# Optimization experiments

Measured on AMD Instinct MI355X. Metric: run time of the kernel, lower is better.

## Reference

```python
import jax, jax.numpy as jnp
import numpy as np

LN_EPS = 1e-5

def _layernorm(x, g, b):
    mu = jnp.mean(x, axis=-1, keepdims=True)
    var = jnp.mean((x - mu) ** 2, axis=-1, keepdims=True)
    return (x - mu) * jax.lax.rsqrt(var + LN_EPS) * g + b

def _mlp(x, w0, b0, wh, bh, lng, lnb, wout, bout):
    # Linear -> ReLU -> LN, repeated; final Linear.
    h = _layernorm(jax.nn.relu(x @ w0.T + b0), lng[0], lnb[0])
    for i in range(wh.shape[0]):
        h = _layernorm(jax.nn.relu(h @ wh[i].T + bh[i]), lng[i + 1], lnb[i + 1])
    return h @ wout.T + bout

def _vq(z, codebook, commitment_cost=0.25):
    B, A, D = z.shape
    flat = z.reshape(-1, D)                                  # [N, D]
    d = (jnp.sum(flat ** 2, axis=1, keepdims=True)
         + jnp.sum(codebook ** 2, axis=1)
         - 2.0 * flat @ codebook.T)                          # [N, K]
    idx = jnp.argmin(d, axis=1)                              # [N]
    quantized = codebook[idx].reshape(z.shape)               # gather, not one-hot matmul
    e_latent = jnp.mean((jax.lax.stop_gradient(quantized) - z) ** 2)
    q_latent = jnp.mean((quantized - jax.lax.stop_gradient(z)) ** 2)
    vq_loss = commitment_cost * e_latent + q_latent
    quantized = z + jax.lax.stop_gradient(quantized - z)     # straight-through
    return quantized, vq_loss

def setup_inputs() -> dict:
    key = jax.random.key(0)
    ks = jax.random.split(key, 8)
    H, D, K = 256, 64, 512
    B, A = 2048, 128
    s = lambda fan_in: 1.0 / np.sqrt(fan_in)
    return {
        'x': jax.random.normal(ks[0], (B, A, 3), jnp.float32),
        'enc_w0': jax.random.normal(ks[1], (H, 3), jnp.float32) * s(3),
        'enc_b0': jnp.zeros((H,), jnp.float32),
        'enc_wh': jax.random.normal(ks[2], (2, H, H), jnp.float32) * s(H),
        'enc_bh': jnp.zeros((2, H), jnp.float32),
        'enc_ln_g': jnp.ones((3, H), jnp.float32),
        'enc_ln_b': jnp.zeros((3, H), jnp.float32),
        'enc_wout': jax.random.normal(ks[3], (D, H), jnp.float32) * s(H),
        'enc_bout': jnp.zeros((D,), jnp.float32),
        'codebook': jax.random.uniform(ks[4], (K, D), jnp.float32, -1.0 / K, 1.0 / K),
        'dec_w0': jax.random.normal(ks[5], (H, D), jnp.float32) * s(D),
        'dec_b0': jnp.zeros((H,), jnp.float32),
        'dec_wh': jax.random.normal(ks[6], (2, H, H), jnp.float32) * s(H),
        'dec_bh': jnp.zeros((2, H), jnp.float32),
        'dec_ln_g': jnp.ones((3, H), jnp.float32),
        'dec_ln_b': jnp.zeros((3, H), jnp.float32),
        'dec_wout': jax.random.normal(ks[7], (3, H), jnp.float32) * s(H),
        'dec_bout': jnp.zeros((3,), jnp.float32),
    }

def reference(x, enc_w0, enc_b0, enc_wh, enc_bh, enc_ln_g, enc_ln_b, enc_wout, enc_bout,
              codebook, dec_w0, dec_b0, dec_wh, dec_bh, dec_ln_g, dec_ln_b, dec_wout, dec_bout):
    z = _mlp(x, enc_w0, enc_b0, enc_wh, enc_bh, enc_ln_g, enc_ln_b, enc_wout, enc_bout)
    quantized, vq_loss = _vq(z, codebook)
    recon = _mlp(quantized, dec_w0, dec_b0, dec_wh, dec_bh, dec_ln_g, dec_ln_b, dec_wout, dec_bout)
    loss = jnp.mean((recon - x) ** 2) + vq_loss
    return recon, quantized, loss
```

## Files before the change

### kernel.cpp

```cpp
#include <hip/hip_runtime.h>
#include <math.h>

__device__ __forceinline__ float wred(float s) {
  #pragma unroll
  for (int o = 32; o > 0; o >>= 1) s += __shfl_xor(s, o, 64);
  return s;
}

__device__ __forceinline__ float fma4(float4 w, float4 a, float acc) {
  return fmaf(w.w, a.w, fmaf(w.z, a.z, fmaf(w.y, a.y, fmaf(w.x, a.x, acc))));
}

__device__ __forceinline__ void ln_rows32(float (*A)[256], const float* __restrict__ gg,
                                          const float* __restrict__ bb, int t) {
  const int w = t >> 6, l = t & 63;
  const float g0 = gg[l], g1 = gg[l + 64], g2 = gg[l + 128], g3 = gg[l + 192];
  const float c0 = bb[l], c1 = bb[l + 64], c2 = bb[l + 128], c3 = bb[l + 192];
  #pragma unroll
  for (int rr = 0; rr < 8; ++rr) {
    const int r = w * 8 + rr;
    const float v0 = A[r][l], v1 = A[r][l + 64], v2 = A[r][l + 128], v3 = A[r][l + 192];
    float s = ((v0 + v1) + v2) + v3;
    s = wred(s);
    const float mu = s * (1.f / 256.f);
    const float d0 = v0 - mu, d1 = v1 - mu, d2 = v2 - mu, d3 = v3 - mu;
    float s2 = fmaf(d3, d3, fmaf(d2, d2, fmaf(d1, d1, d0 * d0)));
    s2 = wred(s2);
    const float var = s2 * (1.f / 256.f);
    const float rs = 1.f / sqrtf(var + 1e-5f);
    A[r][l]       = (d0 * rs) * g0 + c0;
    A[r][l + 64]  = (d1 * rs) * g1 + c1;
    A[r][l + 128] = (d2 * rs) * g2 + c2;
    A[r][l + 192] = (d3 * rs) * g3 + c3;
  }
  __syncthreads();
}

__device__ __forceinline__ void hidden_layer32(float (*A)[256], const float* __restrict__ W,
                                               const float* __restrict__ B, int t) {
  const int g = t >> 7;
  const int j0 = t & 127, j1 = j0 + 128;
  const float4* W0 = (const float4*)(W + j0 * 256);
  const float4* W1 = (const float4*)(W + j1 * 256);
  float acc0[16], acc1[16];
  #pragma unroll
  for (int r = 0; r < 16; ++r) { acc0[r] = 0.f; acc1[r] = 0.f; }
  #pragma unroll 2
  for (int kq = 0; kq < 64; ++kq) {
    const float4 wq0 = W0[kq], wq1 = W1[kq];
    #pragma unroll
    for (int rr = 0; rr < 16; ++rr) {
      const float4 a = *(const float4*)&A[g * 16 + rr][kq * 4];
      acc0[rr] = fma4(wq0, a, acc0[rr]);
      acc1[rr] = fma4(wq1, a, acc1[rr]);
    }
  }
  const float bb0 = B[j0], bb1 = B[j1];
  __syncthreads();
  #pragma unroll
  for (int rr = 0; rr < 16; ++rr) {
    const int r = g * 16 + rr;
    A[r][j0] = fmaxf(acc0[rr] + bb0, 0.f);
    A[r][j1] = fmaxf(acc1[rr] + bb1, 0.f);
  }
  __syncthreads();
}


__device__ __forceinline__ void ldw4(float4* w, const float* __restrict__ WT, int kq, int c0) {
  const float* p = WT + kq * 1024 + c0;
  w[0] = *(const float4*)(p);
  w[1] = *(const float4*)(p + 256);
  w[2] = *(const float4*)(p + 512);
  w[3] = *(const float4*)(p + 768);
}

__device__ __forceinline__ void step16(const float (*A)[256], int kq, const float4* w, float4* acc) {
  #pragma unroll
  for (int rr = 0; rr < 16; ++rr) {
    const float4 a = *(const float4*)&A[rr][kq * 4];
    float4 o = acc[rr];
    o.x = fmaf(a.x, w[0].x, o.x); o.y = fmaf(a.x, w[0].y, o.y);
    o.z = fmaf(a.x, w[0].z, o.z); o.w = fmaf(a.x, w[0].w, o.w);
    o.x = fmaf(a.y, w[1].x, o.x); o.y = fmaf(a.y, w[1].y, o.y);
    o.z = fmaf(a.y, w[1].z, o.z); o.w = fmaf(a.y, w[1].w, o.w);
    o.x = fmaf(a.z, w[2].x, o.x); o.y = fmaf(a.z, w[2].y, o.y);
    o.z = fmaf(a.z, w[2].z, o.z); o.w = fmaf(a.z, w[2].w, o.w);
    o.x = fmaf(a.w, w[3].x, o.x); o.y = fmaf(a.w, w[3].y, o.y);
    o.z = fmaf(a.w, w[3].z, o.z); o.w = fmaf(a.w, w[3].w, o.w);
    acc[rr] = o;
  }
}

__device__ __forceinline__ void hid16(const float (*A)[256], const float* __restrict__ WT,
                                      const float* __restrict__ Bp, int c0, float4* acc) {
  #pragma unroll
  for (int rr = 0; rr < 16; ++rr) acc[rr] = make_float4(0.f, 0.f, 0.f, 0.f);
  float4 wA[4], wB[4];
  ldw4(wA, WT, 0, c0);
  #pragma unroll 1
  for (int kq = 0; kq < 64; kq += 2) {
    ldw4(wB, WT, kq + 1, c0);
    step16(A, kq, wA, acc);
    if (kq + 2 < 64) ldw4(wA, WT, kq + 2, c0);
    step16(A, kq + 1, wB, acc);
  }
  const float4 bb = *(const float4*)&Bp[c0];
  #pragma unroll
  for (int rr = 0; rr < 16; ++rr) {
    acc[rr].x = fmaxf(acc[rr].x + bb.x, 0.f);
    acc[rr].y = fmaxf(acc[rr].y + bb.y, 0.f);
    acc[rr].z = fmaxf(acc[rr].z + bb.z, 0.f);
    acc[rr].w = fmaxf(acc[rr].w + bb.w, 0.f);
  }
}

__device__ __forceinline__ void ln_pad(float4* acc, float (*P)[36],
                                       const float* __restrict__ gg,
                                       const float* __restrict__ bb, int l) {
  const int c0 = l * 4;
  float p[16];
  #pragma unroll
  for (int r = 0; r < 16; ++r) {
    const float4 v = acc[r];
    p[r] = (v.x + v.y) + (v.z + v.w);
  }
  #pragma unroll
  for (int r = 0; r < 16; ++r) p[r] += __shfl_xor(p[r], 32, 64);
  __syncthreads();
  if (l < 32) {
    #pragma unroll
    for (int r = 0; r < 16; ++r) P[r][l] = p[r];
  }
  __syncthreads();
  if (l < 16) {
    float q[8];
    #pragma unroll
    for (int j = 0; j < 8; ++j) {
      const float4 u = *(const float4*)&P[l][4 * j];
      q[j] = (u.x + u.y) + (u.z + u.w);
    }
    const float s = ((q[0] + q[1]) + (q[2] + q[3])) + ((q[4] + q[5]) + (q[6] + q[7]));
    P[l][32] = s * (1.f / 256.f);
  }
  __syncthreads();
  float mu[16];
  #pragma unroll
  for (int r = 0; r < 16; ++r) mu[r] = P[r][32];
  #pragma unroll
  for (int r = 0; r < 16; ++r) {
    const float4 v = acc[r];
    const float d0 = v.x - mu[r], d1 = v.y - mu[r], d2 = v.z - mu[r], d3 = v.w - mu[r];
    p[r] = fmaf(d3, d3, fmaf(d2, d2, fmaf(d1, d1, d0 * d0)));
  }
  #pragma unroll
  for (int r = 0; r < 16; ++r) p[r] += __shfl_xor(p[r], 32, 64);
  if (l < 32) {
    #pragma unroll
    for (int r = 0; r < 16; ++r) P[r][l] = p[r];
  }
  __syncthreads();
  if (l < 16) {
    float q[8];
    #pragma unroll
    for (int j = 0; j < 8; ++j) {
      const float4 u = *(const float4*)&P[l][4 * j];
      q[j] = (u.x + u.y) + (u.z + u.w);
    }
    const float s2 = ((q[0] + q[1]) + (q[2] + q[3])) + ((q[4] + q[5]) + (q[6] + q[7]));
    const float var = s2 * (1.f / 256.f);
    P[l][33] = 1.f / sqrtf(var + 1e-5f);
  }
  __syncthreads();
  const float4 g = *(const float4*)&gg[c0];
  const float4 c = *(const float4*)&bb[c0];
  #pragma unroll
  for (int r = 0; r < 16; ++r) {
    const float rs = P[r][33];
    const float4 v = acc[r];
    acc[r].x = ((v.x - mu[r]) * rs) * g.x + c.x;
    acc[r].y = ((v.y - mu[r]) * rs) * g.y + c.y;
    acc[r].z = ((v.z - mu[r]) * rs) * g.z + c.z;
    acc[r].w = ((v.w - mu[r]) * rs) * g.w + c.w;
  }
}

__device__ __forceinline__ void storeA(float (*A)[256], const float4* acc, int c0) {
  #pragma unroll
  for (int rr = 0; rr < 16; ++rr) *(float4*)&A[rr][c0] = acc[rr];
}

__device__ __forceinline__ void out16(const float (*A)[256], const float* __restrict__ WTo,
                                      const float* __restrict__ bo, float* __restrict__ zout, int l) {
  float o[16];
  #pragma unroll
  for (int rr = 0; rr < 16; ++rr) o[rr] = 0.f;
  #pragma unroll 2
  for (int kq = 0; kq < 64; ++kq) {
    const float w0 = WTo[(kq * 4 + 0) * 64 + l];
    const float w1 = WTo[(kq * 4 + 1) * 64 + l];
    const float w2 = WTo[(kq * 4 + 2) * 64 + l];
    const float w3 = WTo[(kq * 4 + 3) * 64 + l];
    #pragma unroll
    for (int rr = 0; rr < 16; ++rr) {
      const float4 a = *(const float4*)&A[rr][kq * 4];
      o[rr] = fmaf(a.w, w3, fmaf(a.z, w2, fmaf(a.y, w1, fmaf(a.x, w0, o[rr]))));
    }
  }
  const float bb = bo[l];
  #pragma unroll
  for (int rr = 0; rr < 16; ++rr) zout[rr * 64 + l] = o[rr] + bb;
}

__global__ __launch_bounds__(64, 2) void k_enc(
    const float* __restrict__ x, const float* __restrict__ w0,
    const float* __restrict__ b0, const float* __restrict__ wt1,
    const float* __restrict__ wt2, const float* __restrict__ bh,
    const float* __restrict__ lng, const float* __restrict__ lnb,
    const float* __restrict__ wtout, const float* __restrict__ bout,
    float* __restrict__ z) {
  __shared__ float A[16][256];
  __shared__ float P[16][36];
  const int l = threadIdx.x;
  const int c0 = l * 4;
  const size_t rbase = (size_t)blockIdx.x * 16;
  float4 acc[16];

  {
    const float* wp = w0 + c0 * 3;
    float wv[12];
    #pragma unroll
    for (int i = 0; i < 12; ++i) wv[i] = wp[i];
    const float4 bb = *(const float4*)&b0[c0];
    #pragma unroll
    for (int rr = 0; rr < 16; ++rr) {
      const float x0 = x[(rbase + rr) * 3];
      const float x1 = x[(rbase + rr) * 3 + 1];
      const float x2 = x[(rbase + rr) * 3 + 2];
      acc[rr].x = fmaxf(fmaf(wv[2],  x2, fmaf(wv[1],  x1, wv[0] * x0)) + bb.x, 0.f);
      acc[rr].y = fmaxf(fmaf(wv[5],  x2, fmaf(wv[4],  x1, wv[3] * x0)) + bb.y, 0.f);
      acc[rr].z = fmaxf(fmaf(wv[8],  x2, fmaf(wv[7],  x1, wv[6] * x0)) + bb.z, 0.f);
      acc[rr].w = fmaxf(fmaf(wv[11], x2, fmaf(wv[10], x1, wv[9] * x0)) + bb.w, 0.f);
    }
  }
  ln_pad(acc, P, lng, lnb, l);
  storeA(A, acc, c0);
  __syncthreads();

  hid16(A, wt1, bh, c0, acc);
  ln_pad(acc, P, lng + 256, lnb + 256, l);
  storeA(A, acc, c0);
  __syncthreads();

  hid16(A, wt2, bh + 256, c0, acc);
  ln_pad(acc, P, lng + 512, lnb + 512, l);
  storeA(A, acc, c0);
  __syncthreads();

  out16(A, wtout, bout, z + rbase * 64, l);
}

__global__ __launch_bounds__(256) void k_wt(const float* __restrict__ wh,
                                            const float* __restrict__ wout,
                                            float* __restrict__ wt1, float* __restrict__ wt2,
                                            float* __restrict__ wtout) {
  const int b = blockIdx.x, t = threadIdx.x;
  if (b < 256) {
    wt1[b * 256 + t] = wh[t * 256 + b];
  } else if (b < 512) {
    const int k = b - 256;
    wt2[k * 256 + t] = wh[65536 + t * 256 + k];
  } else {
    const int k = (b - 512) * 4 + (t >> 6);
    const int j = t & 63;
    wtout[k * 64 + j] = wout[j * 256 + k];
  }
}

__global__ __launch_bounds__(256) void k_table(
    const float* __restrict__ cb, const float* __restrict__ w0,
    const float* __restrict__ b0, const float* __restrict__ wh,
    const float* __restrict__ bh, const float* __restrict__ lng,
    const float* __restrict__ lnb, const float* __restrict__ wout,
    const float* __restrict__ bout, float* __restrict__ table,
    float* __restrict__ ne) {
  __shared__ float A[32][256];
  __shared__ float cs[32][64];
  const int t = threadIdx.x;
  const int cbase = blockIdx.x * 32;
  {
    float4* d = (float4*)&cs[0][0];
    const float4* s = (const float4*)(cb + cbase * 64);
    d[t] = s[t];
    d[t + 256] = s[t + 256];
  }
  __syncthreads();
  if (t < 32) {
    float s = 0.f;
    #pragma unroll 8
    for (int k = 0; k < 64; ++k) s = fmaf(cs[t][k], cs[t][k], s);
    ne[cbase + t] = s;
  }
  {
    const float4* Wr = (const float4*)(w0 + t * 64);
    float acc[32];
    #pragma unroll
    for (int r = 0; r < 32; ++r) acc[r] = 0.f;
    for (int kq = 0; kq < 16; ++kq) {
      const float4 w = Wr[kq];
      #pragma unroll
      for (int r = 0; r < 32; ++r) {
        const float4 a = *(const float4*)&cs[r][kq * 4];
        acc[r] = fma4(w, a, acc[r]);
      }
    }
    const float bb = b0[t];
    #pragma unroll
    for (int r = 0; r < 32; ++r) A[r][t] = fmaxf(acc[r] + bb, 0.f);
  }
  __syncthreads();
  ln_rows32(A, lng, lnb, t);
  hidden_layer32(A, wh, bh, t);
  ln_rows32(A, lng + 256, lnb + 256, t);
  hidden_layer32(A, wh + 65536, bh + 256, t);
  ln_rows32(A, lng + 512, lnb + 512, t);
  if (t < 96) {
    const int r = t / 3, j = t - r * 3;
    const float4* Wr = (const float4*)(wout + j * 256);
    float s = 0.f;
    #pragma unroll 4
    for (int kq = 0; kq < 64; ++kq) {
      const float4 w = Wr[kq];
      const float4 a = *(const float4*)&A[r][kq * 4];
      s = fma4(w, a, s);
    }
    table[(cbase + r) * 3 + j] = s + bout[j];
  }
}

__global__ __launch_bounds__(256) void k_vq(
    float* __restrict__ zq_io, const float* __restrict__ cb,
    const float* __restrict__ ne, const float* __restrict__ table,
    const float* __restrict__ x, float* __restrict__ recon,
    float* __restrict__ psr, float* __restrict__ psv) {
  __shared__ float red[256];
  const int t = threadIdx.x;
  const int row = blockIdx.x * 256 + t;
  float4 zf[16];
  {
    const float4* zp = (const float4*)(zq_io + (size_t)row * 64);
    #pragma unroll
    for (int q = 0; q < 16; ++q) zf[q] = zp[q];
  }
  float nz = 0.f;
  #pragma unroll
  for (int q = 0; q < 16; ++q) {
    nz = fmaf(zf[q].x, zf[q].x, nz);
    nz = fmaf(zf[q].y, zf[q].y, nz);
    nz = fmaf(zf[q].z, zf[q].z, nz);
    nz = fmaf(zf[q].w, zf[q].w, nz);
  }
  float dmin = INFINITY; int imin = 0;
  const float4* cbv = (const float4*)cb;
  for (int c = 0; c < 512; ++c) {
    float da = 0.f, db = 0.f;
    #pragma unroll
    for (int q = 0; q < 16; q += 2) {
      const float4 ea = cbv[c * 16 + q];
      const float4 eb = cbv[c * 16 + q + 1];
      da = fmaf(ea.x, zf[q].x, da);
      da = fmaf(ea.y, zf[q].y, da);
      da = fmaf(ea.z, zf[q].z, da);
      da = fmaf(ea.w, zf[q].w, da);
      db = fmaf(eb.x, zf[q + 1].x, db);
      db = fmaf(eb.y, zf[q + 1].y, db);
      db = fmaf(eb.z, zf[q + 1].z, db);
      db = fmaf(eb.w, zf[q + 1].w, db);
    }
    const float dot = da + db;
    const float d = (nz + ne[c]) - 2.f * dot;
    if (d < dmin) { dmin = d; imin = c; }
  }
  float sv = 0.f;
  {
    const float4* eq = (const float4*)(cb + imin * 64);
    float4* qo = (float4*)(zq_io + (size_t)row * 64);
    #pragma unroll
    for (int q = 0; q < 16; ++q) {
      const float4 e = eq[q];
      const float4 zz = zf[q];
      const float ax = e.x - zz.x, ay = e.y - zz.y, az = e.z - zz.z, aw = e.w - zz.w;
      sv = fmaf(ax, ax, sv); sv = fmaf(ay, ay, sv);
      sv = fmaf(az, az, sv); sv = fmaf(aw, aw, sv);
      float4 st;
      st.x = zz.x + ax; st.y = zz.y + ay; st.z = zz.z + az; st.w = zz.w + aw;
      qo[q] = st;
    }
  }
  const float r0 = table[imin * 3], r1 = table[imin * 3 + 1], r2 = table[imin * 3 + 2];
  recon[row * 3] = r0; recon[row * 3 + 1] = r1; recon[row * 3 + 2] = r2;
  const float e0 = r0 - x[row * 3], e1 = r1 - x[row * 3 + 1], e2 = r2 - x[row * 3 + 2];
  const float sr = fmaf(e2, e2, fmaf(e1, e1, e0 * e0));
  red[t] = sr; __syncthreads();
  #pragma unroll
  for (int o = 128; o > 0; o >>= 1) { if (t < o) red[t] += red[t + o]; __syncthreads(); }
  if (t == 0) psr[blockIdx.x] = red[0];
  __syncthreads();
  red[t] = sv; __syncthreads();
  #pragma unroll
  for (int o = 128; o > 0; o >>= 1) { if (t < o) red[t] += red[t + o]; __syncthreads(); }
  if (t == 0) psv[blockIdx.x] = red[0];
}

__global__ __launch_bounds__(256) void k_loss(
    const float* __restrict__ psr, const float* __restrict__ psv,
    float* __restrict__ out) {
  __shared__ float ra[256], rb[256];
  const int t = threadIdx.x;
  const float sr = ((psr[t] + psr[t + 256]) + psr[t + 512]) + psr[t + 768];
  const float sv = ((psv[t] + psv[t + 256]) + psv[t + 512]) + psv[t + 768];
  ra[t] = sr; rb[t] = sv;
  __syncthreads();
  #pragma unroll
  for (int o = 128; o > 0; o >>= 1) {
    if (t < o) { ra[t] += ra[t + o]; rb[t] += rb[t + o]; }
    __syncthreads();
  }
  if (t == 0) {
    const float mr = ra[0] / 786432.f;
    const float mv = rb[0] * (1.f / 16777216.f);
    const float vq = 0.25f * mv + mv;
    out[0] = mr + vq;
  }
}

extern "C" void kernel_launch(void* const* d_in, const int* in_sizes, int n_in,
                              void* d_out, int out_size, void* d_ws, size_t ws_size,
                              hipStream_t stream) {
  const float* x        = (const float*)d_in[0];
  const float* enc_w0   = (const float*)d_in[1];
  const float* enc_b0   = (const float*)d_in[2];
  const float* enc_wh   = (const float*)d_in[3];
  const float* enc_bh   = (const float*)d_in[4];
  const float* enc_lng  = (const float*)d_in[5];
  const float* enc_lnb  = (const float*)d_in[6];
  const float* enc_wout = (const float*)d_in[7];
  const float* enc_bout = (const float*)d_in[8];
  const float* cb       = (const float*)d_in[9];
  const float* dec_w0   = (const float*)d_in[10];
  const float* dec_b0   = (const float*)d_in[11];
  const float* dec_wh   = (const float*)d_in[12];
  const float* dec_bh   = (const float*)d_in[13];
  const float* dec_lng  = (const float*)d_in[14];
  const float* dec_lnb  = (const float*)d_in[15];
  const float* dec_wout = (const float*)d_in[16];
  const float* dec_bout = (const float*)d_in[17];

  float* out   = (float*)d_out;
  float* recon = out;
  float* qbuf  = out + 786432;
  float* lossp = out + 786432 + 16777216;

  float* wt1   = out;
  float* wt2   = out + 65536;
  float* wtout = out + 131072;

  float* ws    = (float*)d_ws;
  float* ne    = ws;
  float* table = ws + 512;
  float* psr   = ws + 2048;
  float* psv   = ws + 3072;

  k_wt<<<576, 256, 0, stream>>>(enc_wh, enc_wout, wt1, wt2, wtout);
  k_table<<<16, 256, 0, stream>>>(cb, dec_w0, dec_b0, dec_wh, dec_bh,
                                  dec_lng, dec_lnb, dec_wout, dec_bout,
                                  table, ne);
  k_enc<<<16384, 64, 0, stream>>>(x, enc_w0, enc_b0, wt1, wt2, enc_bh,
                                  enc_lng, enc_lnb, wtout, enc_bout, qbuf);
  k_vq<<<1024, 256, 0, stream>>>(qbuf, cb, ne, table, x, recon, psr, psv);
  k_loss<<<1, 256, 0, stream>>>(psr, psv, lossp);
}
```

Baseline: 1.389 ms.

## Retile encoder kernel to 8x8 register tiles per thread

The encoder kernel's per-thread output tile changes from 16 rows x 4 columns to 8 rows x 8 columns, with each half-wave owning 8 rows. The hidden-layer GEMMs, LayerNorm reduction and output projection are rewritten for this 2D tiling, replacing the cross-half shuffle with shared-memory partial sums. A squarer tile cuts LDS and weight loads per FMA, at the cost of 64 accumulator registers and more barriers in LayerNorm.

```diff
diff --git a/kernel.cpp b/kernel.cpp
--- a/kernel.cpp
+++ b/kernel.cpp
@@ -67,70 +67,17 @@
 }
 
 
-__device__ __forceinline__ void ldw4(float4* w, const float* __restrict__ WT, int kq, int c0) {
-  const float* p = WT + kq * 1024 + c0;
-  w[0] = *(const float4*)(p);
-  w[1] = *(const float4*)(p + 256);
-  w[2] = *(const float4*)(p + 512);
-  w[3] = *(const float4*)(p + 768);
-}
-
-__device__ __forceinline__ void step16(const float (*A)[256], int kq, const float4* w, float4* acc) {
-  #pragma unroll
-  for (int rr = 0; rr < 16; ++rr) {
-    const float4 a = *(const float4*)&A[rr][kq * 4];
-    float4 o = acc[rr];
-    o.x = fmaf(a.x, w[0].x, o.x); o.y = fmaf(a.x, w[0].y, o.y);
-    o.z = fmaf(a.x, w[0].z, o.z); o.w = fmaf(a.x, w[0].w, o.w);
-    o.x = fmaf(a.y, w[1].x, o.x); o.y = fmaf(a.y, w[1].y, o.y);
-    o.z = fmaf(a.y, w[1].z, o.z); o.w = fmaf(a.y, w[1].w, o.w);
-    o.x = fmaf(a.z, w[2].x, o.x); o.y = fmaf(a.z, w[2].y, o.y);
-    o.z = fmaf(a.z, w[2].z, o.z); o.w = fmaf(a.z, w[2].w, o.w);
-    o.x = fmaf(a.w, w[3].x, o.x); o.y = fmaf(a.w, w[3].y, o.y);
-    o.z = fmaf(a.w, w[3].z, o.z); o.w = fmaf(a.w, w[3].w, o.w);
-    acc[rr] = o;
-  }
-}
-
-__device__ __forceinline__ void hid16(const float (*A)[256], const float* __restrict__ WT,
-                                      const float* __restrict__ Bp, int c0, float4* acc) {
-  #pragma unroll
-  for (int rr = 0; rr < 16; ++rr) acc[rr] = make_float4(0.f, 0.f, 0.f, 0.f);
-  float4 wA[4], wB[4];
-  ldw4(wA, WT, 0, c0);
-  #pragma unroll 1
-  for (int kq = 0; kq < 64; kq += 2) {
-    ldw4(wB, WT, kq + 1, c0);
-    step16(A, kq, wA, acc);
-    if (kq + 2 < 64) ldw4(wA, WT, kq + 2, c0);
-    step16(A, kq + 1, wB, acc);
-  }
-  const float4 bb = *(const float4*)&Bp[c0];
-  #pragma unroll
-  for (int rr = 0; rr < 16; ++rr) {
-    acc[rr].x = fmaxf(acc[rr].x + bb.x, 0.f);
-    acc[rr].y = fmaxf(acc[rr].y + bb.y, 0.f);
-    acc[rr].z = fmaxf(acc[rr].z + bb.z, 0.f);
-    acc[rr].w = fmaxf(acc[rr].w + bb.w, 0.f);
-  }
-}
-
-__device__ __forceinline__ void ln_pad(float4* acc, float (*P)[36],
-                                       const float* __restrict__ gg,
-                                       const float* __restrict__ bb, int l) {
-  const int c0 = l * 4;
-  float p[16];
-  #pragma unroll
-  for (int r = 0; r < 16; ++r) {
-    const float4 v = acc[r];
-    p[r] = (v.x + v.y) + (v.z + v.w);
-  }
-  #pragma unroll
-  for (int r = 0; r < 16; ++r) p[r] += __shfl_xor(p[r], 32, 64);
-  __syncthreads();
-  if (l < 32) {
-    #pragma unroll
-    for (int r = 0; r < 16; ++r) P[r][l] = p[r];
+__device__ __forceinline__ void ln64g(float* acc, float (*P)[36],
+                                      const float* __restrict__ gg,
+                                      const float* __restrict__ bb,
+                                      int l, int gr8, int c0) {
+  const int ls = l & 31;
+  float mu[8];
+  #pragma unroll
+  for (int rr = 0; rr < 8; ++rr) {
+    const float* a = &acc[rr * 8];
+    const float s = (((a[0] + a[1]) + (a[2] + a[3])) + ((a[4] + a[5]) + (a[6] + a[7])));
+    P[gr8 + rr][ls] = s;
   }
   __syncthreads();
   if (l < 16) {
@@ -144,20 +91,19 @@
     P[l][32] = s * (1.f / 256.f);
   }
   __syncthreads();
-  float mu[16];
-  #pragma unroll
-  for (int r = 0; r < 16; ++r) mu[r] = P[r][32];
-  #pragma unroll
-  for (int r = 0; r < 16; ++r) {
-    const float4 v = acc[r];
-    const float d0 = v.x - mu[r], d1 = v.y - mu[r], d2 = v.z - mu[r], d3 = v.w - mu[r];
-    p[r] = fmaf(d3, d3, fmaf(d2, d2, fmaf(d1, d1, d0 * d0)));
-  }
-  #pragma unroll
-  for (int r = 0; r < 16; ++r) p[r] += __shfl_xor(p[r], 32, 64);
-  if (l < 32) {
-    #pragma unroll
-    for (int r = 0; r < 16; ++r) P[r][l] = p[r];
+  #pragma unroll
+  for (int rr = 0; rr < 8; ++rr) mu[rr] = P[gr8 + rr][32];
+  __syncthreads();
+  #pragma unroll
+  for (int rr = 0; rr < 8; ++rr) {
+    const float* a = &acc[rr * 8];
+    const float m = mu[rr];
+    const float d0 = a[0] - m, d1 = a[1] - m, d2 = a[2] - m, d3 = a[3] - m;
+    const float d4 = a[4] - m, d5 = a[5] - m, d6 = a[6] - m, d7 = a[7] - m;
+    float s = d0 * d0;
+    s = fmaf(d1, d1, s); s = fmaf(d2, d2, s); s = fmaf(d3, d3, s);
+    s = fmaf(d4, d4, s); s = fmaf(d5, d5, s); s = fmaf(d6, d6, s); s = fmaf(d7, d7, s);
+    P[gr8 + rr][ls] = s;
   }
   __syncthreads();
   if (l < 16) {
@@ -168,48 +114,33 @@
       q[j] = (u.x + u.y) + (u.z + u.w);
     }
     const float s2 = ((q[0] + q[1]) + (q[2] + q[3])) + ((q[4] + q[5]) + (q[6] + q[7]));
-    const float var = s2 * (1.f / 256.f);
-    P[l][33] = 1.f / sqrtf(var + 1e-5f);
-  }
-  __syncthreads();
-  const float4 g = *(const float4*)&gg[c0];
-  const float4 c = *(const float4*)&bb[c0];
-  #pragma unroll
-  for (int r = 0; r < 16; ++r) {
-    const float rs = P[r][33];
-    const float4 v = acc[r];
-    acc[r].x = ((v.x - mu[r]) * rs) * g.x + c.x;
-    acc[r].y = ((v.y - mu[r]) * rs) * g.y + c.y;
-    acc[r].z = ((v.z - mu[r]) * rs) * g.z + c.z;
-    acc[r].w = ((v.w - mu[r]) * rs) * g.w + c.w;
-  }
-}
-
-__device__ __forceinline__ void storeA(float (*A)[256], const float4* acc, int c0) {
-  #pragma unroll
-  for (int rr = 0; rr < 16; ++rr) *(float4*)&A[rr][c0] = acc[rr];
-}
-
-__device__ __forceinline__ void out16(const float (*A)[256], const float* __restrict__ WTo,
-                                      const float* __restrict__ bo, float* __restrict__ zout, int l) {
-  float o[16];
-  #pragma unroll
-  for (int rr = 0; rr < 16; ++rr) o[rr] = 0.f;
-  #pragma unroll 2
-  for (int kq = 0; kq < 64; ++kq) {
-    const float w0 = WTo[(kq * 4 + 0) * 64 + l];
-    const float w1 = WTo[(kq * 4 + 1) * 64 + l];
-    const float w2 = WTo[(kq * 4 + 2) * 64 + l];
-    const float w3 = WTo[(kq * 4 + 3) * 64 + l];
-    #pragma unroll
-    for (int rr = 0; rr < 16; ++rr) {
-      const float4 a = *(const float4*)&A[rr][kq * 4];
-      o[rr] = fmaf(a.w, w3, fmaf(a.z, w2, fmaf(a.y, w1, fmaf(a.x, w0, o[rr]))));
-    }
-  }
-  const float bb = bo[l];
-  #pragma unroll
-  for (int rr = 0; rr < 16; ++rr) zout[rr * 64 + l] = o[rr] + bb;
+    P[l][32] = 1.f / sqrtf(s2 * (1.f / 256.f) + 1e-5f);
+  }
+  __syncthreads();
+  float gv[8], bv[8];
+  *(float4*)&gv[0] = *(const float4*)&gg[c0];
+  *(float4*)&gv[4] = *(const float4*)&gg[c0 + 4];
+  *(float4*)&bv[0] = *(const float4*)&bb[c0];
+  *(float4*)&bv[4] = *(const float4*)&bb[c0 + 4];
+  #pragma unroll
+  for (int rr = 0; rr < 8; ++rr) {
+    const float rs = P[gr8 + rr][32];
+    const float m = mu[rr];
+    #pragma unroll
+    for (int c = 0; c < 8; ++c)
+      acc[rr * 8 + c] = ((acc[rr * 8 + c] - m) * rs) * gv[c] + bv[c];
+  }
+  __syncthreads();
+}
+
+__device__ __forceinline__ void storeA64g(float (*A)[256], const float* acc, int gr8, int c0) {
+  #pragma unroll
+  for (int rr = 0; rr < 8; ++rr) {
+    *(float4*)&A[gr8 + rr][c0] =
+        make_float4(acc[rr * 8], acc[rr * 8 + 1], acc[rr * 8 + 2], acc[rr * 8 + 3]);
+    *(float4*)&A[gr8 + rr][c0 + 4] =
+        make_float4(acc[rr * 8 + 4], acc[rr * 8 + 5], acc[rr * 8 + 6], acc[rr * 8 + 7]);
+  }
 }
 
 __global__ __launch_bounds__(64, 2) void k_enc(
@@ -222,42 +153,122 @@
   __shared__ float A[16][256];
   __shared__ float P[16][36];
   const int l = threadIdx.x;
-  const int c0 = l * 4;
+  const int gr8 = (l >> 5) * 8;
+  const int c0 = (l & 31) * 8;
   const size_t rbase = (size_t)blockIdx.x * 16;
-  float4 acc[16];
-
-  {
-    const float* wp = w0 + c0 * 3;
-    float wv[12];
-    #pragma unroll
-    for (int i = 0; i < 12; ++i) wv[i] = wp[i];
-    const float4 bb = *(const float4*)&b0[c0];
-    #pragma unroll
-    for (int rr = 0; rr < 16; ++rr) {
-      const float x0 = x[(rbase + rr) * 3];
-      const float x1 = x[(rbase + rr) * 3 + 1];
-      const float x2 = x[(rbase + rr) * 3 + 2];
-      acc[rr].x = fmaxf(fmaf(wv[2],  x2, fmaf(wv[1],  x1, wv[0] * x0)) + bb.x, 0.f);
-      acc[rr].y = fmaxf(fmaf(wv[5],  x2, fmaf(wv[4],  x1, wv[3] * x0)) + bb.y, 0.f);
-      acc[rr].z = fmaxf(fmaf(wv[8],  x2, fmaf(wv[7],  x1, wv[6] * x0)) + bb.z, 0.f);
-      acc[rr].w = fmaxf(fmaf(wv[11], x2, fmaf(wv[10], x1, wv[9] * x0)) + bb.w, 0.f);
-    }
-  }
-  ln_pad(acc, P, lng, lnb, l);
-  storeA(A, acc, c0);
-  __syncthreads();
-
-  hid16(A, wt1, bh, c0, acc);
-  ln_pad(acc, P, lng + 256, lnb + 256, l);
-  storeA(A, acc, c0);
-  __syncthreads();
-
-  hid16(A, wt2, bh + 256, c0, acc);
-  ln_pad(acc, P, lng + 512, lnb + 512, l);
-  storeA(A, acc, c0);
-  __syncthreads();
-
-  out16(A, wtout, bout, z + rbase * 64, l);
+  float acc[64];
+
+  {
+    float wv[24], bv[8];
+    #pragma unroll
+    for (int i = 0; i < 6; ++i) *(float4*)&wv[i * 4] = *(const float4*)&w0[c0 * 3 + i * 4];
+    *(float4*)&bv[0] = *(const float4*)&b0[c0];
+    *(float4*)&bv[4] = *(const float4*)&b0[c0 + 4];
+    #pragma unroll
+    for (int rr = 0; rr < 8; ++rr) {
+      const size_t r3 = (rbase + gr8 + rr) * 3;
+      const float x0 = x[r3], x1 = x[r3 + 1], x2 = x[r3 + 2];
+      #pragma unroll
+      for (int c = 0; c < 8; ++c) {
+        const float s = fmaf(wv[c * 3 + 2], x2, fmaf(wv[c * 3 + 1], x1, wv[c * 3] * x0));
+        acc[rr * 8 + c] = fmaxf(s + bv[c], 0.f);
+      }
+    }
+  }
+  ln64g(acc, P, lng, lnb, l, gr8, c0);
+  storeA64g(A, acc, gr8, c0);
+  __syncthreads();
+
+  #pragma unroll 1
+  for (int layer = 0; layer < 2; ++layer) {
+    const float* __restrict__ WT = layer == 0 ? wt1 : wt2;
+    const float* __restrict__ Bp = layer == 0 ? bh : bh + 256;
+
+    #define LDWQ(buf, kqv) { \
+      _Pragma("unroll") \
+      for (int kk_ = 0; kk_ < 4; ++kk_) { \
+        buf[kk_ * 2]     = *(const float4*)&WT[(size_t)((kqv) * 4 + kk_) * 256 + c0]; \
+        buf[kk_ * 2 + 1] = *(const float4*)&WT[(size_t)((kqv) * 4 + kk_) * 256 + c0 + 4]; \
+      } }
+    #define QUADF(kqv, wbuf) { \
+      float4 a_[8]; \
+      _Pragma("unroll") \
+      for (int i_ = 0; i_ < 8; ++i_) a_[i_] = *(const float4*)&A[gr8 + i_][(kqv) * 4]; \
+      _Pragma("unroll") \
+      for (int kk_ = 0; kk_ < 4; ++kk_) { \
+        const float4 wlo_ = wbuf[kk_ * 2], whi_ = wbuf[kk_ * 2 + 1]; \
+        _Pragma("unroll") \
+        for (int i_ = 0; i_ < 8; ++i_) { \
+          const float av_ = kk_ == 0 ? a_[i_].x : kk_ == 1 ? a_[i_].y : kk_ == 2 ? a_[i_].z : a_[i_].w; \
+          acc[i_ * 8 + 0] = fmaf(av_, wlo_.x, acc[i_ * 8 + 0]); \
+          acc[i_ * 8 + 1] = fmaf(av_, wlo_.y, acc[i_ * 8 + 1]); \
+          acc[i_ * 8 + 2] = fmaf(av_, wlo_.z, acc[i_ * 8 + 2]); \
+          acc[i_ * 8 + 3] = fmaf(av_, wlo_.w, acc[i_ * 8 + 3]); \
+          acc[i_ * 8 + 4] = fmaf(av_, whi_.x, acc[i_ * 8 + 4]); \
+          acc[i_ * 8 + 5] = fmaf(av_, whi_.y, acc[i_ * 8 + 5]); \
+          acc[i_ * 8 + 6] = fmaf(av_, whi_.z, acc[i_ * 8 + 6]); \
+          acc[i_ * 8 + 7] = fmaf(av_, whi_.w, acc[i_ * 8 + 7]); \
+        } } }
+
+    #pragma unroll
+    for (int i = 0; i < 64; ++i) acc[i] = 0.f;
+    float4 wA[8], wB[8];
+    LDWQ(wA, 0);
+    #pragma unroll 1
+    for (int kq = 0; kq < 64; kq += 2) {
+      LDWQ(wB, kq + 1);
+      QUADF(kq, wA);
+      if (kq + 2 < 64) LDWQ(wA, kq + 2);
+      QUADF(kq + 1, wB);
+    }
+    #undef LDWQ
+    #undef QUADF
+    {
+      float bv[8];
+      *(float4*)&bv[0] = *(const float4*)&Bp[c0];
+      *(float4*)&bv[4] = *(const float4*)&Bp[c0 + 4];
+      #pragma unroll
+      for (int rr = 0; rr < 8; ++rr)
+        #pragma unroll
+        for (int c = 0; c < 8; ++c)
+          acc[rr * 8 + c] = fmaxf(acc[rr * 8 + c] + bv[c], 0.f);
+    }
+    ln64g(acc, P, lng + 256 + layer * 256, lnb + 256 + layer * 256, l, gr8, c0);
+    __syncthreads();
+    storeA64g(A, acc, gr8, c0);
+    __syncthreads();
+  }
+
+  {
+    const int c0o = (l & 31) * 2;
+    float o[16];
+    #pragma unroll
+    for (int i = 0; i < 16; ++i) o[i] = 0.f;
+    #pragma unroll 1
+    for (int kq = 0; kq < 64; ++kq) {
+      float4 a[8];
+      #pragma unroll
+      for (int i = 0; i < 8; ++i) a[i] = *(const float4*)&A[gr8 + i][kq * 4];
+      #pragma unroll
+      for (int kk = 0; kk < 4; ++kk) {
+        const float2 wv = *(const float2*)&wtout[(size_t)(kq * 4 + kk) * 64 + c0o];
+        #pragma unroll
+        for (int i = 0; i < 8; ++i) {
+          const float av = kk == 0 ? a[i].x : kk == 1 ? a[i].y : kk == 2 ? a[i].z : a[i].w;
+          o[i * 2]     = fmaf(av, wv.x, o[i * 2]);
+          o[i * 2 + 1] = fmaf(av, wv.y, o[i * 2 + 1]);
+        }
+      }
+    }
+    const float2 bb = *(const float2*)&bout[c0o];
+    #pragma unroll
+    for (int rr = 0; rr < 8; ++rr) {
+      float2 st;
+      st.x = o[rr * 2] + bb.x;
+      st.y = o[rr * 2 + 1] + bb.y;
+      *(float2*)&z[(rbase + gr8 + rr) * 64 + c0o] = st;
+    }
+  }
 }
 
 __global__ __launch_bounds__(256) void k_wt(const float* __restrict__ wh,
```

Measured after the change: 1.357 ms. 2.3% less time.
